# Kernel tuning notes

Hardware: AMD Instinct MI355X
Metric: run time of the kernel (lower is better)

Reference implementation:

```python
import jax, jax.numpy as jnp
import numpy as np
from jax import lax

B, L, T = 16, 512, 128
V, D = 21128, 512


def setup_inputs() -> dict:
    key = jax.random.key(0)
    ks = jax.random.split(key, 24)
    s = 0.05
    p = lambda k, shape: jax.random.normal(k, shape, jnp.float32) * s
    return {
        'document_input_ids': jax.random.randint(ks[0], (B, L), 0, V),
        'summary_input_ids': jax.random.randint(ks[1], (B, T), 0, V),
        'E': p(ks[2], (V, D)),
        'Wih_f': p(ks[3], (4 * D, D)), 'Whh_f': p(ks[4], (4 * D, D)),
        'bih_f': p(ks[5], (4 * D,)), 'bhh_f': p(ks[6], (4 * D,)),
        'Wih_b': p(ks[7], (4 * D, D)), 'Whh_b': p(ks[8], (4 * D, D)),
        'bih_b': p(ks[9], (4 * D,)), 'bhh_b': p(ks[10], (4 * D,)),
        'fc_W': p(ks[11], (D, 2 * D)), 'fc_b': p(ks[12], (D,)),
        'attn_W': p(ks[13], (D, 3 * D)), 'attn_b': p(ks[14], (D,)),
        'v_w': p(ks[15], (D,)),
        'dWih': p(ks[16], (4 * D, 3 * D)),
        'dbih': p(ks[17], (4 * D,)), 'dbhh': p(ks[18], (4 * D,)),
        'dfc_W': p(ks[19], (V, 4 * D)), 'dfc_b': p(ks[20], (V,)),
    }


def _lstm_dir(x, Wih, Whh, bih, bhh, reverse):
    # x: (B, L, Din) -> outputs (B, L, D) plus final hidden (B, D)
    xg = jnp.einsum('bld,gd->blg', x, Wih) + bih + bhh  # precompute input gates

    def step(carry, xt):
        h, c = carry
        g = xt + h @ Whh.T
        i, f, gg, o = jnp.split(g, 4, axis=-1)  # PyTorch gate order i,f,g,o
        i = jax.nn.sigmoid(i); f = jax.nn.sigmoid(f)
        gg = jnp.tanh(gg); o = jax.nn.sigmoid(o)
        c = f * c + i * gg
        h = o * jnp.tanh(c)
        return (h, c), h

    h0 = jnp.zeros((x.shape[0], Whh.shape[1]), x.dtype)
    (hT, _), hs = lax.scan(step, (h0, h0), jnp.swapaxes(xg, 0, 1), reverse=reverse)
    return jnp.swapaxes(hs, 0, 1), hT


def reference(document_input_ids, summary_input_ids, E,
              Wih_f, Whh_f, bih_f, bhh_f,
              Wih_b, Whh_b, bih_b, bhh_b,
              fc_W, fc_b, attn_W, attn_b, v_w,
              dWih, dbih, dbhh, dfc_W, dfc_b):
    # --- encoder (BiLSTM over document; dropout is identity at eval) ---
    emb = E[document_input_ids]                       # (B, L, D)
    enc_f, h_f = _lstm_dir(emb, Wih_f, Whh_f, bih_f, bhh_f, reverse=False)
    enc_b, h_b = _lstm_dir(emb, Wih_b, Whh_b, bih_b, bhh_b, reverse=True)
    enc = jnp.concatenate([enc_f, enc_b], axis=-1)    # (B, L, 2D)
    hidden = jnp.tanh(jnp.concatenate([h_f, h_b], axis=-1) @ fc_W.T + fc_b)  # (B, D)

    # --- Bahdanau attention, computed once (as in the original forward) ---
    bsz, dlen = enc.shape[0], enc.shape[1]
    hrep = jnp.broadcast_to(hidden[:, None, :], (bsz, dlen, hidden.shape[-1]))
    energy = jnp.tanh(jnp.concatenate([hrep, enc], axis=2) @ attn_W.T + attn_b)
    att = energy @ v_w                                 # (B, L)
    mask = document_input_ids != 0
    att = jnp.where(mask, att, jnp.float32(-1e10))
    a = jax.nn.softmax(att, axis=1)
    weighted = jnp.einsum('bl,ble->be', a, enc)        # (B, 2D), constant over steps

    # --- decoder: teacher forcing; d_lstm gets a fresh zero state each step,
    # so all T-1 steps are independent and fully vectorized ---
    toks = summary_input_ids[:, :-1]                   # inputs for t = 1..T-1
    emb_s = E[toks]                                    # (B, T-1, D)
    w_b = jnp.broadcast_to(weighted[:, None, :], (bsz, toks.shape[1], weighted.shape[-1]))
    x = jnp.concatenate([emb_s, w_b], axis=2)          # (B, T-1, 3D)
    g = jnp.einsum('btd,gd->btg', x, dWih) + dbih + dbhh
    i, f, gg, o = jnp.split(g, 4, axis=-1)
    c = jax.nn.sigmoid(i) * jnp.tanh(gg)               # h_prev = c_prev = 0
    h = jax.nn.sigmoid(o) * jnp.tanh(c)                # (B, T-1, D)
    pred = jnp.einsum('btd,vd->btv', jnp.concatenate([h, w_b, emb_s], axis=2), dfc_W) + dfc_b
    logits = jnp.concatenate([jnp.zeros((bsz, 1, pred.shape[-1]), pred.dtype), pred], axis=1)
    logits = jnp.transpose(logits, (0, 2, 1))          # (B, V, T) as in the torch code

    # --- CrossEntropyLoss over all positions (incl. the zero-logit t=0) ---
    logp = jax.nn.log_softmax(logits, axis=1)
    nll = -jnp.take_along_axis(logp, summary_input_ids[:, None, :], axis=1).squeeze(1)
    loss = nll.mean()
    return logits, loss
```

## Files before the change

### kernel.cpp

```cpp
#include <hip/hip_runtime.h>
#include <math.h>

typedef __attribute__((ext_vector_type(8))) short bf16x8;
typedef __attribute__((ext_vector_type(4))) float f32x4;
typedef unsigned int u32;
typedef unsigned short u16;
typedef unsigned long long u64;

#define BB 16
#define LL 512
#define TT 128
#define VV 21128
#define DD 512

__device__ __forceinline__ float b2f(u16 h){ return __uint_as_float(((u32)h) << 16); }
__device__ __forceinline__ u16 f2bf(float x){
    u32 u = __float_as_uint(x);
    return (u16)((u + 0x7fffu + ((u >> 16) & 1u)) >> 16);
}
__device__ __forceinline__ float sigf(float x){ return 1.0f / (1.0f + __expf(-x)); }
__device__ __forceinline__ bf16x8 pack8(float4 a, float4 b){
    bf16x8 r;
    r[0]=(short)f2bf(a.x); r[1]=(short)f2bf(a.y); r[2]=(short)f2bf(a.z); r[3]=(short)f2bf(a.w);
    r[4]=(short)f2bf(b.x); r[5]=(short)f2bf(b.y); r[6]=(short)f2bf(b.z); r[7]=(short)f2bf(b.w);
    return r;
}

__global__ void kz(u32* p, int n){
    int i = blockIdx.x * 256 + threadIdx.x;
    if (i < n) p[i] = 0u;
}

__global__ void k_embed(const int* __restrict__ doc, const float* __restrict__ E,
                        u16* __restrict__ emb2){
    int r = blockIdx.x;
    int lane = threadIdx.x;
    int l = r >> 4, b = r & 15;
    int tok = doc[b * LL + l];
    const float* src = E + (size_t)tok * DD + lane * 8;
    float4 a = *(const float4*)(src);
    float4 c = *(const float4*)(src + 4);
    *(bf16x8*)(emb2 + (size_t)r * DD + lane * 8) = pack8(a, c);
}

template<int MODE>
__global__ __launch_bounds__(256) void k_gemm(
    const u16* __restrict__ A, const float* __restrict__ Bt, void* __restrict__ Out,
    const float* __restrict__ b1, const float* __restrict__ b2, int M, int N, int K)
{
    __shared__ u16 smem[17408];
    u16* sA = smem;
    u16* sB = smem + 128 * 56;
    int tid = threadIdx.x;
    int nb = blockIdx.x, mb = blockIdx.y;
    int wv = tid >> 6, lane = tid & 63;
    int wm = wv >> 1, wn = wv & 1;
    int lrow = lane & 15, quad = lane >> 4;
    f32x4 acc[4][4] = {};
    int kt_n = K >> 5;
    for (int kt = 0; kt < kt_n; ++kt){
        int k0 = kt << 5;
        bf16x8 va[2];
        u64 qb[4];
        #pragma unroll
        for (int h = 0; h < 2; ++h){
            int c = tid + (h << 8);
            int row = c >> 2, c4 = c & 3;
            va[h] = *(const bf16x8*)(A + (size_t)(mb * 128 + row) * K + k0 + c4 * 8);
        }
        #pragma unroll
        for (int h = 0; h < 4; ++h){
            int c = tid + (h << 8);
            int row = c >> 3, seg = c & 7;
            int rb = nb * 128 + row; rb = rb < N ? rb : N - 1;
            float4 v = *(const float4*)(Bt + (size_t)rb * K + k0 + seg * 4);
            qb[h] = (u64)f2bf(v.x) | ((u64)f2bf(v.y) << 16) |
                    ((u64)f2bf(v.z) << 32) | ((u64)f2bf(v.w) << 48);
        }
        __syncthreads();
        #pragma unroll
        for (int h = 0; h < 2; ++h){
            int c = tid + (h << 8);
            int row = c >> 2, c4 = c & 3;
            *(bf16x8*)(sA + row * 56 + c4 * 8) = va[h];
        }
        #pragma unroll
        for (int h = 0; h < 4; ++h){
            int c = tid + (h << 8);
            int row = c >> 3, seg = c & 7;
            *(u64*)(sB + row * 56 + seg * 4) = qb[h];
        }
        __syncthreads();
        bf16x8 af[4], bfr[4];
        #pragma unroll
        for (int i = 0; i < 4; ++i){
            af[i]  = *(const bf16x8*)(sA + (wm * 64 + i * 16 + lrow) * 56 + quad * 8);
            bfr[i] = *(const bf16x8*)(sB + (wn * 64 + i * 16 + lrow) * 56 + quad * 8);
        }
        #pragma unroll
        for (int i = 0; i < 4; ++i)
            #pragma unroll
            for (int j = 0; j < 4; ++j)
                acc[i][j] = __builtin_amdgcn_mfma_f32_16x16x32_bf16(af[i], bfr[j], acc[i][j], 0, 0, 0);
    }

    if (MODE == 0 || MODE == 1){
        u16* O = (u16*)Out;
        #pragma unroll
        for (int i = 0; i < 4; ++i){
            int rowb = mb * 128 + wm * 64 + i * 16 + quad * 4;
            #pragma unroll
            for (int j = 0; j < 4; ++j){
                int col = nb * 128 + wn * 64 + j * 16 + lrow;
                float bias = b1[col] + (b2 ? b2[col] : 0.0f);
                #pragma unroll
                for (int r = 0; r < 4; ++r){
                    float v = acc[i][j][r] + bias;
                    if (MODE == 1) v = tanhf(v);
                    O[(size_t)(rowb + r) * N + col] = f2bf(v);
                }
            }
        }
    } else {
        float* Of = (float*)Out;
        float* lds_f = (float*)smem;
        #pragma unroll
        for (int h = 0; h < 2; ++h){
            __syncthreads();
            if (wn == h){
                #pragma unroll
                for (int j = 0; j < 4; ++j){
                    int nl = j * 16 + lrow;
                    int vg = nb * 128 + h * 64 + nl;
                    float bias = (vg < VV) ? b1[vg] : 0.0f;
                    #pragma unroll
                    for (int i = 0; i < 4; ++i){
                        #pragma unroll
                        for (int r = 0; r < 4; ++r){
                            int tl = wm * 64 + i * 16 + quad * 4 + r;
                            lds_f[nl * 132 + tl] = (tl == 0) ? 0.0f : (acc[i][j][r] + bias);
                        }
                    }
                }
            }
            __syncthreads();
            int vloc = tid >> 2, seg = tid & 3;
            int ng = nb * 128 + h * 64 + vloc;
            if (ng < VV){
                float4* dst = (float4*)(Of + ((size_t)mb * VV + ng) * TT + seg * 32);
                const float4* src = (const float4*)(lds_f + vloc * 132 + seg * 32);
                #pragma unroll
                for (int q = 0; q < 8; ++q) dst[q] = src[q];
            }
        }
    }
}

__global__ __launch_bounds__(256, 1) void k_lstm(
    const u16* __restrict__ xg_f, const u16* __restrict__ xg_b,
    const float* __restrict__ Whh_f, const float* __restrict__ Whh_b,
    u16* __restrict__ hist_f, u16* __restrict__ hist_b,
    u32* __restrict__ hbuf, u32* __restrict__ flags)
{
    int tid = threadIdx.x;
    int wv = tid >> 6, lane = tid & 63;
    int blk = blockIdx.x;
    int dir = blk >> 3;
    int w = ((blk & 7) << 2) + wv;
    int d0 = w << 4;
    int lrow = lane & 15, quad = lane >> 4;

    const u16* xg  = dir ? xg_b : xg_f;
    const float* Whh = dir ? Whh_b : Whh_f;
    u16* hist = dir ? hist_b : hist_f;
    u32* myflag = flags + (((dir << 5) + w) << 5);
    u32* pflag  = flags + (((dir << 5) + (lane & 31)) << 5);

    bf16x8 bfr[4][16];
    #pragma unroll
    for (int g = 0; g < 4; ++g){
        const float* wp = Whh + (size_t)((g << 9) + d0 + lrow) * DD;
        #pragma unroll
        for (int kb = 0; kb < 16; ++kb){
            float4 x0 = *(const float4*)(wp + kb * 32 + quad * 8);
            float4 x1 = *(const float4*)(wp + kb * 32 + quad * 8 + 4);
            bfr[g][kb] = pack8(x0, x1);
        }
    }
    float c_reg[4] = {0.0f, 0.0f, 0.0f, 0.0f};

    for (int s = 0; s < LL; ++s){
        int t = dir ? (LL - 1 - s) : s;
        int rp = s & 1;
        u32* hb_r = hbuf + ((dir * 2 + rp) << 12);
        u32* hb_w = hbuf + ((dir * 2 + (rp ^ 1)) << 12);

        u16 xv[4][4];
        const u16* xgp = xg + (size_t)(t << 4) * 2048 + d0 + lrow;
        #pragma unroll
        for (int g = 0; g < 4; ++g)
            #pragma unroll
            for (int r = 0; r < 4; ++r)
                xv[g][r] = xgp[(size_t)((quad << 2) + r) * 2048 + (g << 9)];

        if (s){
            u32 tgt = (u32)s;
            while (1){
                u32 v = __hip_atomic_load(pflag, __ATOMIC_ACQUIRE, __HIP_MEMORY_SCOPE_AGENT);
                if (__all((int)(v >= tgt))) break;
                __builtin_amdgcn_s_sleep(1);
            }
        }

        u64* hrow = (u64*)(hb_r + (lrow << 8));
        bf16x8 af[16];
        #pragma unroll
        for (int kb = 0; kb < 16; ++kb){
            union { u64 q[2]; bf16x8 v; } u;
            u.q[0] = __hip_atomic_load(hrow + kb * 8 + quad * 2,     __ATOMIC_RELAXED, __HIP_MEMORY_SCOPE_AGENT);
            u.q[1] = __hip_atomic_load(hrow + kb * 8 + quad * 2 + 1, __ATOMIC_RELAXED, __HIP_MEMORY_SCOPE_AGENT);
            af[kb] = u.v;
        }

        f32x4 acc[4] = {};
        #pragma unroll
        for (int kb = 0; kb < 16; ++kb){
            #pragma unroll
            for (int g = 0; g < 4; ++g)
                acc[g] = __builtin_amdgcn_mfma_f32_16x16x32_bf16(af[kb], bfr[g][kb], acc[g], 0, 0, 0);
        }

        #pragma unroll
        for (int r = 0; r < 4; ++r){
            float gi = acc[0][r] + b2f(xv[0][r]);
            float gf = acc[1][r] + b2f(xv[1][r]);
            float gg = acc[2][r] + b2f(xv[2][r]);
            float go = acc[3][r] + b2f(xv[3][r]);
            float cv = sigf(gf) * c_reg[r] + sigf(gi) * tanhf(gg);
            c_reg[r] = cv;
            u32 me = (u32)f2bf(sigf(go) * tanhf(cv));
            u32 ot = __shfl_xor(me, 1);
            if (!(lane & 1)){
                u32 uw = me | (ot << 16);
                int batch = (quad << 2) + r;
                __hip_atomic_store(hb_w + (batch << 8) + ((d0 + lrow) >> 1), uw,
                                   __ATOMIC_RELAXED, __HIP_MEMORY_SCOPE_AGENT);
                *(u32*)(hist + (size_t)((t << 4) + batch) * DD + d0 + lrow) = uw;
            }
        }
        if (lane == 0)
            __hip_atomic_store(myflag, (u32)(s + 1), __ATOMIC_RELEASE, __HIP_MEMORY_SCOPE_AGENT);
    }
}

__global__ void k_fc(const u16* __restrict__ hist_f, const u16* __restrict__ hist_b,
                     const float* __restrict__ fcW, const float* __restrict__ fcB,
                     u16* __restrict__ hidden){
    int idx = blockIdx.x * 256 + threadIdx.x;
    int b = idx >> 9, n = idx & 511;
    const u16* hf = hist_f + (size_t)(511 * 16 + b) * DD;
    const u16* hb = hist_b + (size_t)b * DD;
    const float* w = fcW + (size_t)n * 1024;
    float sacc = 0.0f;
    for (int k = 0; k < 512; ++k) sacc += b2f(hf[k]) * w[k];
    for (int k = 0; k < 512; ++k) sacc += b2f(hb[k]) * w[512 + k];
    hidden[b * 512 + n] = f2bf(tanhf(sacc + fcB[n]));
}

__global__ void k_packatt(const u16* __restrict__ hidden, const u16* __restrict__ hist_f,
                          const u16* __restrict__ hist_b, u16* __restrict__ X){
    int r = blockIdx.x;
    int b = r >> 9, l = r & 511;
    u16* xr = X + (size_t)r * 1536;
    const u16* hf = hist_f + (size_t)(l * 16 + b) * DD;
    const u16* hb = hist_b + (size_t)(l * 16 + b) * DD;
    const u16* hd = hidden + b * 512;
    for (int j = threadIdx.x; j < 512; j += 256){
        xr[j] = hd[j];
        xr[512 + j] = hf[j];
        xr[1024 + j] = hb[j];
    }
}

__global__ void k_att(const u16* __restrict__ energy, const float* __restrict__ vw,
                      const int* __restrict__ doc, float* __restrict__ att){
    int r = blockIdx.x * 4 + (threadIdx.x >> 6);
    int lane = threadIdx.x & 63;
    bf16x8 e = *(const bf16x8*)(energy + (size_t)r * 512 + lane * 8);
    float4 v0 = *(const float4*)(vw + lane * 8);
    float4 v1 = *(const float4*)(vw + lane * 8 + 4);
    float sacc = b2f((u16)e[0]) * v0.x + b2f((u16)e[1]) * v0.y +
                 b2f((u16)e[2]) * v0.z + b2f((u16)e[3]) * v0.w +
                 b2f((u16)e[4]) * v1.x + b2f((u16)e[5]) * v1.y +
                 b2f((u16)e[6]) * v1.z + b2f((u16)e[7]) * v1.w;
    #pragma unroll
    for (int o = 1; o < 64; o <<= 1) sacc += __shfl_xor(sacc, o);
    if (lane == 0){
        int b = r >> 9, l = r & 511;
        att[r] = (doc[b * 512 + l] != 0) ? sacc : -1e10f;
    }
}

__global__ __launch_bounds__(256) void k_smw(const float* __restrict__ att,
                                             const u16* __restrict__ hist_f,
                                             const u16* __restrict__ hist_b,
                                             float* __restrict__ weighted){
    __shared__ float sa[512];
    __shared__ float red[256];
    int b = blockIdx.x, tid = threadIdx.x;
    float a0 = att[b * 512 + tid], a1 = att[b * 512 + 256 + tid];
    red[tid] = fmaxf(a0, a1); __syncthreads();
    for (int o = 128; o > 0; o >>= 1){ if (tid < o) red[tid] = fmaxf(red[tid], red[tid + o]); __syncthreads(); }
    float mx = red[0]; __syncthreads();
    float e0 = __expf(a0 - mx), e1 = __expf(a1 - mx);
    red[tid] = e0 + e1; __syncthreads();
    for (int o = 128; o > 0; o >>= 1){ if (tid < o) red[tid] += red[tid + o]; __syncthreads(); }
    float inv = 1.0f / red[0];
    sa[tid] = e0 * inv; sa[256 + tid] = e1 * inv;
    __syncthreads();
    #pragma unroll
    for (int ch = 0; ch < 4; ++ch){
        int e = (ch << 8) + tid;
        const u16* src = (e < 512) ? (hist_f + b * DD + e) : (hist_b + b * DD + (e - 512));
        float acc = 0.0f;
        for (int l = 0; l < 512; ++l) acc += sa[l] * b2f(src[(size_t)l * 16 * DD]);
        weighted[b * 1024 + e] = acc;
    }
}

__global__ void k_packdec(const int* __restrict__ sids, const float* __restrict__ E,
                          const float* __restrict__ weighted,
                          u16* __restrict__ X_dec, u16* __restrict__ X_pred){
    int r = blockIdx.x;
    int b = r >> 7, t = r & 127;
    u16* xd = X_dec + (size_t)r * 1536;
    u16* xp = X_pred + (size_t)r * 2048;
    const float* er = (t > 0) ? (E + (size_t)sids[b * 128 + t - 1] * DD) : (const float*)0;
    for (int j = threadIdx.x; j < 512; j += 256){
        u16 v = (t > 0) ? f2bf(er[j]) : (u16)0;
        xd[j] = v; xp[1536 + j] = v;
    }
    for (int j = threadIdx.x; j < 1024; j += 256){
        u16 wv = f2bf(weighted[b * 1024 + j]);
        xd[512 + j] = wv; xp[512 + j] = wv;
    }
}

__global__ void k_gate(const u16* __restrict__ g, u16* __restrict__ X_pred){
    int idx = blockIdx.x * 256 + threadIdx.x;
    int r = idx >> 9, d = idx & 511;
    const u16* gr = g + (size_t)r * 2048;
    float gi = b2f(gr[d]), gg = b2f(gr[1024 + d]), go = b2f(gr[1536 + d]);
    float c = sigf(gi) * tanhf(gg);
    X_pred[(size_t)r * 2048 + d] = f2bf(sigf(go) * tanhf(c));
}

__global__ void k_lossp(const float* __restrict__ out, float* __restrict__ part){
    int b = blockIdx.x >> 5, ch = blockIdx.x & 31;
    int t = threadIdx.x;
    int v0 = ch * 661, v1 = v0 + 661; if (v1 > VV) v1 = VV;
    const float* col = out + (size_t)b * VV * TT + t;
    float m = -1e30f, sacc = 0.0f;
    for (int v = v0; v < v1; ++v){
        float x = col[(size_t)v * TT];
        float nm = fmaxf(m, x);
        sacc = sacc * __expf(m - nm) + __expf(x - nm);
        m = nm;
    }
    float2* p = (float2*)part;
    p[((b * 32 + ch) << 7) + t] = make_float2(m, sacc);
}

__global__ __launch_bounds__(256) void k_lossm(const float* __restrict__ part,
                                               const float* __restrict__ out,
                                               const int* __restrict__ sids,
                                               float* __restrict__ loss_out){
    __shared__ float red[256];
    int tid = threadIdx.x;
    float local = 0.0f;
    #pragma unroll
    for (int p8 = 0; p8 < 8; ++p8){
        int pair = (p8 << 8) + tid;
        int b = pair >> 7, t = pair & 127;
        const float2* pp = (const float2*)part + ((size_t)(b * 32) << 7) + t;
        float M = -1e30f;
        for (int c = 0; c < 32; ++c) M = fmaxf(M, pp[c << 7].x);
        float S = 0.0f;
        for (int c = 0; c < 32; ++c){ float2 q = pp[c << 7]; S += q.y * __expf(q.x - M); }
        float logZ = M + __logf(S);
        int tgt = sids[b * 128 + t];
        float x = out[(size_t)b * VV * TT + (size_t)tgt * TT + t];
        local += (logZ - x);
    }
    red[tid] = local; __syncthreads();
    for (int o = 128; o > 0; o >>= 1){ if (tid < o) red[tid] += red[tid + o]; __syncthreads(); }
    if (tid == 0) loss_out[0] = red[0] / 2048.0f;
}

extern "C" void kernel_launch(void* const* d_in, const int* in_sizes, int n_in,
                              void* d_out, int out_size, void* d_ws, size_t ws_size,
                              hipStream_t stream)
{
    const int*   doc  = (const int*)d_in[0];
    const int*   sids = (const int*)d_in[1];
    const float* E    = (const float*)d_in[2];
    const float* WihF = (const float*)d_in[3];
    const float* WhhF = (const float*)d_in[4];
    const float* bihF = (const float*)d_in[5];
    const float* bhhF = (const float*)d_in[6];
    const float* WihB = (const float*)d_in[7];
    const float* WhhB = (const float*)d_in[8];
    const float* bihB = (const float*)d_in[9];
    const float* bhhB = (const float*)d_in[10];
    const float* fcW  = (const float*)d_in[11];
    const float* fcB  = (const float*)d_in[12];
    const float* attW = (const float*)d_in[13];
    const float* attB = (const float*)d_in[14];
    const float* vw   = (const float*)d_in[15];
    const float* dWih = (const float*)d_in[16];
    const float* dbih = (const float*)d_in[17];
    const float* dbhh = (const float*)d_in[18];
    const float* dfcW = (const float*)d_in[19];
    const float* dfcB = (const float*)d_in[20];
    float* out = (float*)d_out;

    char* ws = (char*)d_ws;
    const size_t EMB2 = 0;
    const size_t XG   = EMB2 + 8388608ull;
    const size_t XGB  = XG   + 33554432ull;
    const size_t HHF  = XGB  + 33554432ull;
    const size_t HHB  = HHF  + 8388608ull;
    const size_t HBUF = HHB  + 8388608ull;
    const size_t HID  = HBUF + 66560ull;
    const size_t FLG  = 0;
    const size_t XATT = XG;
    const size_t ENER = XATT + 25165824ull;
    const size_t ATT  = ENER + 8388608ull;
    const size_t WEI  = ATT  + 32768ull;
    const size_t XDEC = WEI  + 65536ull;
    const size_t GDEC = XDEC + 6291456ull;
    const size_t XPRD = GDEC + 8388608ull;
    const size_t PART = XPRD + 8388608ull;

    u16* emb2  = (u16*)(ws + EMB2);
    u16* xgf   = (u16*)(ws + XG);
    u16* xgb   = (u16*)(ws + XGB);
    u16* hhf   = (u16*)(ws + HHF);
    u16* hhb   = (u16*)(ws + HHB);
    u32* hbuf  = (u32*)(ws + HBUF);
    u32* flags = (u32*)(ws + FLG);
    u16* hid   = (u16*)(ws + HID);
    u16* xatt  = (u16*)(ws + XATT);
    u16* ener  = (u16*)(ws + ENER);
    float* att = (float*)(ws + ATT);
    float* wei = (float*)(ws + WEI);
    u16* xdec  = (u16*)(ws + XDEC);
    u16* gdec  = (u16*)(ws + GDEC);
    u16* xprd  = (u16*)(ws + XPRD);
    float* part= (float*)(ws + PART);

    (void)in_sizes; (void)n_in; (void)out_size; (void)ws_size;

    kz<<<dim3(64), dim3(256), 0, stream>>>(hbuf, 16384);
    k_embed<<<dim3(8192), dim3(64), 0, stream>>>(doc, E, emb2);
    k_gemm<0><<<dim3(16, 64), dim3(256), 0, stream>>>(emb2, WihF, (void*)xgf, bihF, bhhF, 8192, 2048, 512);
    k_gemm<0><<<dim3(16, 64), dim3(256), 0, stream>>>(emb2, WihB, (void*)xgb, bihB, bhhB, 8192, 2048, 512);
    kz<<<dim3(8), dim3(256), 0, stream>>>(flags, 2048);
    k_lstm<<<dim3(16), dim3(256), 0, stream>>>(xgf, xgb, WhhF, WhhB, hhf, hhb, hbuf, flags);
    k_fc<<<dim3(32), dim3(256), 0, stream>>>(hhf, hhb, fcW, fcB, hid);
    k_packatt<<<dim3(8192), dim3(256), 0, stream>>>(hid, hhf, hhb, xatt);
    k_gemm<1><<<dim3(4, 64), dim3(256), 0, stream>>>(xatt, attW, (void*)ener, attB, (const float*)0, 8192, 512, 1536);
    k_att<<<dim3(2048), dim3(256), 0, stream>>>(ener, vw, doc, att);
    k_smw<<<dim3(16), dim3(256), 0, stream>>>(att, hhf, hhb, wei);
    k_packdec<<<dim3(2048), dim3(256), 0, stream>>>(sids, E, wei, xdec, xprd);
    k_gemm<0><<<dim3(16, 16), dim3(256), 0, stream>>>(xdec, dWih, (void*)gdec, dbih, dbhh, 2048, 2048, 1536);
    k_gate<<<dim3(4096), dim3(256), 0, stream>>>(gdec, xprd);
    k_gemm<2><<<dim3(166, 16), dim3(256), 0, stream>>>(xprd, dfcW, (void*)out, dfcB, (const float*)0, 2048, 21128, 2048);
    k_lossp<<<dim3(512), dim3(128), 0, stream>>>(out, part);
    k_lossm<<<dim3(1), dim3(256), 0, stream>>>(part, out, sids, out + (size_t)BB * VV * TT);
}
```

Measured before the change: 5.759 ms.

## Replace LSTM flag barrier with per-element step tags in hidden-state buffer

```diff
diff --git a/kernel.cpp b/kernel.cpp
--- a/kernel.cpp
+++ b/kernel.cpp
@@ -26,9 +26,9 @@
     return r;
 }
 
-__global__ void kz(u32* p, int n){
+__global__ void k_init(u32* hb){
     int i = blockIdx.x * 256 + threadIdx.x;
-    if (i < n) p[i] = 0u;
+    hb[i] = ((i >> 13) & 1) ? 0u : 1u;
 }
 
 __global__ void k_embed(const int* __restrict__ doc, const float* __restrict__ E,
@@ -160,7 +160,7 @@
     const u16* __restrict__ xg_f, const u16* __restrict__ xg_b,
     const float* __restrict__ Whh_f, const float* __restrict__ Whh_b,
     u16* __restrict__ hist_f, u16* __restrict__ hist_b,
-    u32* __restrict__ hbuf, u32* __restrict__ flags)
+    u32* __restrict__ hbuf)
 {
     int tid = threadIdx.x;
     int wv = tid >> 6, lane = tid & 63;
@@ -173,8 +173,7 @@
     const u16* xg  = dir ? xg_b : xg_f;
     const float* Whh = dir ? Whh_b : Whh_f;
     u16* hist = dir ? hist_b : hist_f;
-    u32* myflag = flags + (((dir << 5) + w) << 5);
-    u32* pflag  = flags + (((dir << 5) + (lane & 31)) << 5);
+    u32* hb_base = hbuf + (dir << 14);
 
     bf16x8 bfr[4][16];
     #pragma unroll
@@ -191,9 +190,11 @@
 
     for (int s = 0; s < LL; ++s){
         int t = dir ? (LL - 1 - s) : s;
-        int rp = s & 1;
-        u32* hb_r = hbuf + ((dir * 2 + rp) << 12);
-        u32* hb_w = hbuf + ((dir * 2 + (rp ^ 1)) << 12);
+        u32* hb_r = hb_base + ((s & 1) << 13);
+        u32* hb_w = hb_base + (((s + 1) & 1) << 13);
+        u32 tagr = (u32)(s + 1);
+        u32 tagtag = tagr | (tagr << 16);
+        u32 tagw = (u32)(s + 2);
 
         u16 xv[4][4];
         const u16* xgp = xg + (size_t)(t << 4) * 2048 + d0 + lrow;
@@ -202,32 +203,37 @@
             #pragma unroll
             for (int r = 0; r < 4; ++r)
                 xv[g][r] = xgp[(size_t)((quad << 2) + r) * 2048 + (g << 9)];
-
-        if (s){
-            u32 tgt = (u32)s;
-            while (1){
-                u32 v = __hip_atomic_load(pflag, __ATOMIC_ACQUIRE, __HIP_MEMORY_SCOPE_AGENT);
-                if (__all((int)(v >= tgt))) break;
-                __builtin_amdgcn_s_sleep(1);
-            }
-        }
-
-        u64* hrow = (u64*)(hb_r + (lrow << 8));
-        bf16x8 af[16];
+        __builtin_amdgcn_sched_barrier(0);
+
+        const u64* hrow = (const u64*)hb_r + (lrow << 8) + (quad << 2);
+        u64 wd[64];
+        while (1){
+            #pragma unroll
+            for (int q = 0; q < 64; ++q)
+                wd[q] = __hip_atomic_load(hrow + ((q >> 2) << 4) + (q & 3),
+                                          __ATOMIC_RELAXED, __HIP_MEMORY_SCOPE_AGENT);
+            u32 orr = 0;
+            #pragma unroll
+            for (int q = 0; q < 64; ++q){
+                u32 lo = (u32)wd[q], hi = (u32)(wd[q] >> 32);
+                orr |= __builtin_amdgcn_perm(hi, lo, 0x05040100u) ^ tagtag;
+            }
+            if (__all(orr == 0)) break;
+            __builtin_amdgcn_s_sleep(1);
+        }
+
+        f32x4 acc[4] = {};
         #pragma unroll
         for (int kb = 0; kb < 16; ++kb){
-            union { u64 q[2]; bf16x8 v; } u;
-            u.q[0] = __hip_atomic_load(hrow + kb * 8 + quad * 2,     __ATOMIC_RELAXED, __HIP_MEMORY_SCOPE_AGENT);
-            u.q[1] = __hip_atomic_load(hrow + kb * 8 + quad * 2 + 1, __ATOMIC_RELAXED, __HIP_MEMORY_SCOPE_AGENT);
-            af[kb] = u.v;
-        }
-
-        f32x4 acc[4] = {};
-        #pragma unroll
-        for (int kb = 0; kb < 16; ++kb){
+            union { bf16x8 v; u32 u[4]; } af;
+            #pragma unroll
+            for (int m = 0; m < 4; ++m){
+                u64 x = wd[(kb << 2) + m];
+                af.u[m] = __builtin_amdgcn_perm((u32)(x >> 32), (u32)x, 0x07060302u);
+            }
             #pragma unroll
             for (int g = 0; g < 4; ++g)
-                acc[g] = __builtin_amdgcn_mfma_f32_16x16x32_bf16(af[kb], bfr[g][kb], acc[g], 0, 0, 0);
+                acc[g] = __builtin_amdgcn_mfma_f32_16x16x32_bf16(af.v, bfr[g][kb], acc[g], 0, 0, 0);
         }
 
         #pragma unroll
@@ -239,17 +245,14 @@
             float cv = sigf(gf) * c_reg[r] + sigf(gi) * tanhf(gg);
             c_reg[r] = cv;
             u32 me = (u32)f2bf(sigf(go) * tanhf(cv));
+            int batch = (quad << 2) + r;
+            __hip_atomic_store(hb_w + (batch << 9) + d0 + lrow, (me << 16) | tagw,
+                               __ATOMIC_RELAXED, __HIP_MEMORY_SCOPE_AGENT);
             u32 ot = __shfl_xor(me, 1);
             if (!(lane & 1)){
-                u32 uw = me | (ot << 16);
-                int batch = (quad << 2) + r;
-                __hip_atomic_store(hb_w + (batch << 8) + ((d0 + lrow) >> 1), uw,
-                                   __ATOMIC_RELAXED, __HIP_MEMORY_SCOPE_AGENT);
-                *(u32*)(hist + (size_t)((t << 4) + batch) * DD + d0 + lrow) = uw;
-            }
-        }
-        if (lane == 0)
-            __hip_atomic_store(myflag, (u32)(s + 1), __ATOMIC_RELEASE, __HIP_MEMORY_SCOPE_AGENT);
+                *(u32*)(hist + (size_t)((t << 4) + batch) * DD + d0 + lrow) = me | (ot << 16);
+            }
+        }
     }
 }
 
@@ -432,7 +435,6 @@
     const size_t HHB  = HHF  + 8388608ull;
     const size_t HBUF = HHB  + 8388608ull;
     const size_t HID  = HBUF + 66560ull;
-    const size_t FLG  = 0;
     const size_t XATT = XG;
     const size_t ENER = XATT + 25165824ull;
     const size_t ATT  = ENER + 8388608ull;
@@ -447,8 +449,7 @@
     u16* xgb   = (u16*)(ws + XGB);
     u16* hhf   = (u16*)(ws + HHF);
     u16* hhb   = (u16*)(ws + HHB);
-    u32* hbuf  = (u32*)(ws + HBUF);
-    u32* flags = (u32*)(ws + FLG);
+    u32* hbuf  = (u32*)(ws + EMB2);
     u16* hid   = (u16*)(ws + HID);
     u16* xatt  = (u16*)(ws + XATT);
     u16* ener  = (u16*)(ws + ENER);
@@ -461,12 +462,11 @@
 
     (void)in_sizes; (void)n_in; (void)out_size; (void)ws_size;
 
-    kz<<<dim3(64), dim3(256), 0, stream>>>(hbuf, 16384);
     k_embed<<<dim3(8192), dim3(64), 0, stream>>>(doc, E, emb2);
     k_gemm<0><<<dim3(16, 64), dim3(256), 0, stream>>>(emb2, WihF, (void*)xgf, bihF, bhhF, 8192, 2048, 512);
     k_gemm<0><<<dim3(16, 64), dim3(256), 0, stream>>>(emb2, WihB, (void*)xgb, bihB, bhhB, 8192, 2048, 512);
-    kz<<<dim3(8), dim3(256), 0, stream>>>(flags, 2048);
-    k_lstm<<<dim3(16), dim3(256), 0, stream>>>(xgf, xgb, WhhF, WhhB, hhf, hhb, hbuf, flags);
+    k_init<<<dim3(128), dim3(256), 0, stream>>>(hbuf);
+    k_lstm<<<dim3(16), dim3(256), 0, stream>>>(xgf, xgb, WhhF, WhhB, hhf, hhb, hbuf);
     k_fc<<<dim3(32), dim3(256), 0, stream>>>(hhf, hhb, fcW, fcB, hid);
     k_packatt<<<dim3(8192), dim3(256), 0, stream>>>(hid, hhf, hhb, xatt);
     k_gemm<1><<<dim3(4, 64), dim3(256), 0, stream>>>(xatt, attW, (void*)ener, attB, (const float*)0, 8192, 512, 1536);
```

After: 8.556 ms. 48.6% more time.

## Tighten LSTM inter-block step synchronization and move history stores off critical path

Applied to the files above, without the earlier changes.

```diff
diff --git a/kernel.cpp b/kernel.cpp
--- a/kernel.cpp
+++ b/kernel.cpp
@@ -173,8 +173,9 @@
     const u16* xg  = dir ? xg_b : xg_f;
     const float* Whh = dir ? Whh_b : Whh_f;
     u16* hist = dir ? hist_b : hist_f;
-    u32* myflag = flags + (((dir << 5) + w) << 5);
-    u32* pflag  = flags + (((dir << 5) + (lane & 31)) << 5);
+    u32* hb_base = hbuf + (dir << 13);
+    u32* myflag = flags + (dir << 5) + w;
+    const u32* pflag = flags + (dir << 5) + (lane & 31);
 
     bf16x8 bfr[4][16];
     #pragma unroll
@@ -191,9 +192,8 @@
 
     for (int s = 0; s < LL; ++s){
         int t = dir ? (LL - 1 - s) : s;
-        int rp = s & 1;
-        u32* hb_r = hbuf + ((dir * 2 + rp) << 12);
-        u32* hb_w = hbuf + ((dir * 2 + (rp ^ 1)) << 12);
+        u32* hb_r = hb_base + ((s & 1) << 12);
+        u32* hb_w = hb_base + (((s + 1) & 1) << 12);
 
         u16 xv[4][4];
         const u16* xgp = xg + (size_t)(t << 4) * 2048 + d0 + lrow;
@@ -202,17 +202,18 @@
             #pragma unroll
             for (int r = 0; r < 4; ++r)
                 xv[g][r] = xgp[(size_t)((quad << 2) + r) * 2048 + (g << 9)];
+        __builtin_amdgcn_sched_barrier(0);
 
         if (s){
             u32 tgt = (u32)s;
             while (1){
-                u32 v = __hip_atomic_load(pflag, __ATOMIC_ACQUIRE, __HIP_MEMORY_SCOPE_AGENT);
+                u32 v = __hip_atomic_load(pflag, __ATOMIC_RELAXED, __HIP_MEMORY_SCOPE_AGENT);
                 if (__all((int)(v >= tgt))) break;
-                __builtin_amdgcn_s_sleep(1);
             }
         }
-
-        u64* hrow = (u64*)(hb_r + (lrow << 8));
+        __builtin_amdgcn_sched_barrier(0);
+
+        const u64* hrow = (const u64*)(hb_r + (lrow << 8));
         bf16x8 af[16];
         #pragma unroll
         for (int kb = 0; kb < 16; ++kb){
@@ -230,6 +231,7 @@
                 acc[g] = __builtin_amdgcn_mfma_f32_16x16x32_bf16(af[kb], bfr[g][kb], acc[g], 0, 0, 0);
         }
 
+        u32 hw[4]; int hb_ok[4];
         #pragma unroll
         for (int r = 0; r < 4; ++r){
             float gi = acc[0][r] + b2f(xv[0][r]);
@@ -240,16 +242,22 @@
             c_reg[r] = cv;
             u32 me = (u32)f2bf(sigf(go) * tanhf(cv));
             u32 ot = __shfl_xor(me, 1);
+            u32 uw = me | (ot << 16);
+            int batch = (quad << 2) + r;
+            hw[r] = uw; hb_ok[r] = batch;
             if (!(lane & 1)){
-                u32 uw = me | (ot << 16);
-                int batch = (quad << 2) + r;
                 __hip_atomic_store(hb_w + (batch << 8) + ((d0 + lrow) >> 1), uw,
                                    __ATOMIC_RELAXED, __HIP_MEMORY_SCOPE_AGENT);
-                *(u32*)(hist + (size_t)((t << 4) + batch) * DD + d0 + lrow) = uw;
             }
         }
+        asm volatile("s_waitcnt vmcnt(0)" ::: "memory");
         if (lane == 0)
-            __hip_atomic_store(myflag, (u32)(s + 1), __ATOMIC_RELEASE, __HIP_MEMORY_SCOPE_AGENT);
+            __hip_atomic_store(myflag, (u32)(s + 1), __ATOMIC_RELAXED, __HIP_MEMORY_SCOPE_AGENT);
+        #pragma unroll
+        for (int r = 0; r < 4; ++r){
+            if (!(lane & 1))
+                *(u32*)(hist + (size_t)((t << 4) + hb_ok[r]) * DD + d0 + lrow) = hw[r];
+        }
     }
 }
 
@@ -432,7 +440,6 @@
     const size_t HHB  = HHF  + 8388608ull;
     const size_t HBUF = HHB  + 8388608ull;
     const size_t HID  = HBUF + 66560ull;
-    const size_t FLG  = 0;
     const size_t XATT = XG;
     const size_t ENER = XATT + 25165824ull;
     const size_t ATT  = ENER + 8388608ull;
@@ -447,8 +454,8 @@
     u16* xgb   = (u16*)(ws + XGB);
     u16* hhf   = (u16*)(ws + HHF);
     u16* hhb   = (u16*)(ws + HHB);
-    u32* hbuf  = (u32*)(ws + HBUF);
-    u32* flags = (u32*)(ws + FLG);
+    u32* hbuf  = (u32*)(ws + EMB2);
+    u32* flags = hbuf + 16384;
     u16* hid   = (u16*)(ws + HID);
     u16* xatt  = (u16*)(ws + XATT);
     u16* ener  = (u16*)(ws + ENER);
@@ -461,11 +468,10 @@
 
     (void)in_sizes; (void)n_in; (void)out_size; (void)ws_size;
 
-    kz<<<dim3(64), dim3(256), 0, stream>>>(hbuf, 16384);
     k_embed<<<dim3(8192), dim3(64), 0, stream>>>(doc, E, emb2);
     k_gemm<0><<<dim3(16, 64), dim3(256), 0, stream>>>(emb2, WihF, (void*)xgf, bihF, bhhF, 8192, 2048, 512);
     k_gemm<0><<<dim3(16, 64), dim3(256), 0, stream>>>(emb2, WihB, (void*)xgb, bihB, bhhB, 8192, 2048, 512);
-    kz<<<dim3(8), dim3(256), 0, stream>>>(flags, 2048);
+    kz<<<dim3(65), dim3(256), 0, stream>>>(hbuf, 16448);
     k_lstm<<<dim3(16), dim3(256), 0, stream>>>(xgf, xgb, WhhF, WhhB, hhf, hhb, hbuf, flags);
     k_fc<<<dim3(32), dim3(256), 0, stream>>>(hhf, hhb, fcW, fcB, hid);
     k_packatt<<<dim3(8192), dim3(256), 0, stream>>>(hid, hhf, hhb, xatt);
```

After: 4.864 ms. -15.5%, faster.
